# Kernel optimization log

Hardware: AMD Instinct MI355X
Metric: run time of the kernel (lower is better)

The kernel has to match this reference:

```python
import jax, jax.numpy as jnp
import numpy as np

B, S, D, H = 4, 2048, 1024, 16
HD = D // H
FF = 4 * D
EPS = 1e-5


def setup_inputs() -> dict:
    key = jax.random.key(0)
    ks = jax.random.split(key, 12)
    s = lambda fan_in: 1.0 / np.sqrt(fan_in)
    inp = {
        "x": jax.random.normal(ks[0], (B, S, D), dtype=jnp.float32),
        # attention weights stored as (d_in, d_out)
        "Wq": jax.random.normal(ks[1], (D, D), dtype=jnp.float32) * s(D),
        "Wk": jax.random.normal(ks[2], (D, D), dtype=jnp.float32) * s(D),
        "Wv": jax.random.normal(ks[3], (D, D), dtype=jnp.float32) * s(D),
        "Wo": jax.random.normal(ks[4], (D, D), dtype=jnp.float32) * s(D),
        "bo": jnp.zeros((D,), dtype=jnp.float32),
        # feed-forward
        "W1": jax.random.normal(ks[5], (D, FF), dtype=jnp.float32) * s(D),
        "b1": jnp.zeros((FF,), dtype=jnp.float32),
        "W2": jax.random.normal(ks[6], (FF, D), dtype=jnp.float32) * s(FF),
        "b2": jnp.zeros((D,), dtype=jnp.float32),
        # layernorms
        "g1": jnp.ones((D,), dtype=jnp.float32),
        "be1": jnp.zeros((D,), dtype=jnp.float32),
        "g2": jnp.ones((D,), dtype=jnp.float32),
        "be2": jnp.zeros((D,), dtype=jnp.float32),
    }
    return inp


def _layernorm(x, gamma, beta):
    mean = jnp.mean(x, axis=-1, keepdims=True)
    var = jnp.mean(jnp.square(x - mean), axis=-1, keepdims=True)  # unbiased=False
    return gamma * (x - mean) / jnp.sqrt(var + EPS) + beta


def _gelu_tanh(x):
    c = jnp.sqrt(jnp.asarray(2.0 / jnp.pi, dtype=x.dtype))
    return 0.5 * x * (1.0 + jnp.tanh(c * (x + 0.044715 * x * x * x)))


def _block(x, Wq, Wk, Wv, Wo, bo, W1, b1, W2, b2, g1, be1, g2, be2):
    # --- pre-LN causal multi-head attention ---
    shortcut = x
    h = _layernorm(x, g1, be1)
    q = (h @ Wq).reshape(B, S, H, HD).transpose(0, 2, 1, 3)  # [B,H,S,HD]
    k = (h @ Wk).reshape(B, S, H, HD).transpose(0, 2, 1, 3)
    v = (h @ Wv).reshape(B, S, H, HD).transpose(0, 2, 1, 3)
    scores = jnp.einsum("bhqd,bhkd->bhqk", q, k)
    causal = jnp.tril(jnp.ones((S, S), dtype=bool))  # True = keep
    scores = jnp.where(causal, scores, -jnp.inf)
    attn = jax.nn.softmax(scores / jnp.sqrt(jnp.asarray(HD, scores.dtype)), axis=-1)
    ctx = jnp.einsum("bhqk,bhkd->bqhd", attn, v).reshape(B, S, D)
    x = ctx @ Wo + bo + shortcut
    # --- pre-LN GELU MLP ---
    shortcut = x
    h = _layernorm(x, g2, be2)
    h = _gelu_tanh(h @ W1 + b1) @ W2 + b2
    return h + shortcut


def reference(x, Wq, Wk, Wv, Wo, bo, W1, b1, W2, b2, g1, be1, g2, be2):
    return _block(x, Wq, Wk, Wv, Wo, bo, W1, b1, W2, b2, g1, be1, g2, be2)
```

## Files before the change

### kernel.cpp

```cpp
#include <hip/hip_runtime.h>
#include <cstdint>

#define B_   4
#define S_   2048
#define D_   1024
#define H_   16
#define HD_  64
#define FF_  4096
#define MTOK 8192

typedef short s16x8 __attribute__((ext_vector_type(8), may_alias));
typedef float f32x4 __attribute__((ext_vector_type(4)));
typedef unsigned short u16x4 __attribute__((ext_vector_type(4), may_alias));
typedef unsigned short u16x8 __attribute__((ext_vector_type(8), may_alias));

#define GLD_LDS16(g, l)                                                  \
  __builtin_amdgcn_global_load_lds(                                      \
      (__attribute__((address_space(1))) void*)(g),                      \
      (__attribute__((address_space(3))) void*)(l), 16, 0, 0)

__device__ __forceinline__ unsigned short f2bf(float f) {
  unsigned u = __float_as_uint(f);
  unsigned r = 0x7fffu + ((u >> 16) & 1u);
  return (unsigned short)((u + r) >> 16);
}

__global__ __launch_bounds__(256) void k_transpose(const float* __restrict__ in,
                                                   unsigned short* __restrict__ out,
                                                   int R, int C) {
  __shared__ float tile[32][33];
  int tx = threadIdx.x, ty = threadIdx.y;
  int c0 = blockIdx.x * 32, r0 = blockIdx.y * 32;
#pragma unroll
  for (int j = 0; j < 4; ++j)
    tile[ty + j * 8][tx] = in[(size_t)(r0 + ty + j * 8) * C + (c0 + tx)];
  __syncthreads();
#pragma unroll
  for (int j = 0; j < 4; ++j)
    out[(size_t)(c0 + ty + j * 8) * R + (r0 + tx)] = f2bf(tile[tx][ty + j * 8]);
}

__global__ __launch_bounds__(256) void k_layernorm(const float* __restrict__ x,
                                                   const float* __restrict__ g,
                                                   const float* __restrict__ be,
                                                   unsigned short* __restrict__ out) {
  int row = blockIdx.x, t = threadIdx.x;
  const float4* xr = (const float4*)(x + (size_t)row * D_);
  float4 v = xr[t];
  float s = v.x + v.y + v.z + v.w;
  float q = v.x * v.x + v.y * v.y + v.z * v.z + v.w * v.w;
#pragma unroll
  for (int o = 1; o < 64; o <<= 1) { s += __shfl_xor(s, o); q += __shfl_xor(q, o); }
  __shared__ float red[8];
  int wid = t >> 6;
  if ((t & 63) == 0) { red[wid * 2] = s; red[wid * 2 + 1] = q; }
  __syncthreads();
  s = red[0] + red[2] + red[4] + red[6];
  q = red[1] + red[3] + red[5] + red[7];
  float mean = s * (1.0f / D_);
  float rstd = rsqrtf(q * (1.0f / D_) - mean * mean + 1e-5f);
  float4 gv = ((const float4*)g)[t];
  float4 bv = ((const float4*)be)[t];
  u16x4 o4;
  o4[0] = f2bf(gv.x * (v.x - mean) * rstd + bv.x);
  o4[1] = f2bf(gv.y * (v.y - mean) * rstd + bv.y);
  o4[2] = f2bf(gv.z * (v.z - mean) * rstd + bv.z);
  o4[3] = f2bf(gv.w * (v.w - mean) * rstd + bv.w);
  *(u16x4*)(out + (size_t)row * D_ + t * 4) = o4;
}

template <int MODE>
__global__ __launch_bounds__(512, 2) void k_gemm8p(
    const unsigned short* __restrict__ A, const unsigned short* __restrict__ Bt,
    const float* __restrict__ bias,
    unsigned short* __restrict__ outb,
    int M, int N, int K) {
  __shared__ __align__(16) unsigned short smem[8 * 8192];
  unsigned short* const Rs = smem;

  const int tid = threadIdx.x;
  const int wid = tid >> 6, lane = tid & 63;
  const int l16 = lane & 15, lg = lane >> 4;
  const int wr = wid >> 2, wc = wid & 3;
  const int nwg = gridDim.x * gridDim.y;
  const int id = blockIdx.y * gridDim.x + blockIdx.x;
  const int swz = (id & 7) * (nwg >> 3) + (id >> 3);
  const int m0 = (swz / gridDim.x) * 256, n0 = (swz % gridDim.x) * 256;

  f32x4 acc[8][4];
#pragma unroll
  for (int m = 0; m < 8; ++m)
#pragma unroll
    for (int n = 0; n < 4; ++n) acc[m][n] = (f32x4)0.0f;

  const int sRow = tid >> 3;
  const int sC = (((tid & 7) ^ (sRow & 7)) << 3);
  const unsigned short* aS0 = A + (size_t)(m0 + sRow) * K + sC;
  const unsigned short* aS1 = A + (size_t)(m0 + 64 + sRow) * K + sC;
  const unsigned short* aS2 = A + (size_t)(m0 + 128 + sRow) * K + sC;
  const unsigned short* aS3 = A + (size_t)(m0 + 192 + sRow) * K + sC;
  const unsigned short* bS0 = Bt + (size_t)(n0 + sRow) * K + sC;
  const unsigned short* bS1 = Bt + (size_t)(n0 + 64 + sRow) * K + sC;
  const unsigned short* bS2 = Bt + (size_t)(n0 + 128 + sRow) * K + sC;
  const unsigned short* bS3 = Bt + (size_t)(n0 + 192 + sRow) * K + sC;
  const int d0 = tid * 16, d1 = tid * 16 + 8192;

  const int cS0 = ((lg ^ (l16 & 7)) << 3);
  const int cS1 = (((4 + lg) ^ (l16 & 7)) << 3);

#define READ_A(SLOT)                                                           \
  _Pragma("unroll")                                                            \
  for (int m4 = 0; m4 < 4; ++m4) {                                             \
    const unsigned short* pr_ = smem + (SLOT) * 8192 + (wr * 64 + m4 * 16 + l16) * 64; \
    af[m4][0] = *(const s16x8*)(pr_ + cS0);                                    \
    af[m4][1] = *(const s16x8*)(pr_ + cS1);                                    \
  }
#define READ_B(SLOT, DEST)                                                     \
  _Pragma("unroll")                                                            \
  for (int n2 = 0; n2 < 2; ++n2) {                                             \
    const unsigned short* pr_ = smem + (SLOT) * 8192 + (wc * 32 + n2 * 16 + l16) * 64; \
    DEST[n2][0] = *(const s16x8*)(pr_ + cS0);                                  \
    DEST[n2][1] = *(const s16x8*)(pr_ + cS1);                                  \
  }
#define STAGE2(SLOT, P0_, P1_, KOFF)                                           \
  {                                                                            \
    char* dst_ = (char*)(smem + (SLOT) * 8192);                                \
    GLD_LDS16((P0_) + (KOFF), dst_ + d0);                                      \
    GLD_LDS16((P1_) + (KOFF), dst_ + d1);                                      \
  }
#define MFMAQ(MQ, NH, AF, BF)                                                  \
  __builtin_amdgcn_s_setprio(1);                                               \
  _Pragma("unroll")                                                            \
  for (int m4 = 0; m4 < 4; ++m4)                                               \
    _Pragma("unroll")                                                          \
    for (int n2 = 0; n2 < 2; ++n2) {                                           \
      acc[(MQ) * 4 + m4][(NH) * 2 + n2] = __builtin_amdgcn_mfma_f32_16x16x32_bf16( \
          AF[m4][0], BF[n2][0], acc[(MQ) * 4 + m4][(NH) * 2 + n2], 0, 0, 0);   \
      acc[(MQ) * 4 + m4][(NH) * 2 + n2] = __builtin_amdgcn_mfma_f32_16x16x32_bf16( \
          AF[m4][1], BF[n2][1], acc[(MQ) * 4 + m4][(NH) * 2 + n2], 0, 0, 0);   \
    }                                                                          \
  __builtin_amdgcn_s_setprio(0);
#define LGK0                                                                   \
  asm volatile("s_waitcnt lgkmcnt(0)" ::: "memory");                           \
  __builtin_amdgcn_sched_barrier(0);
#define BAR_ONLY                                                               \
  __builtin_amdgcn_sched_barrier(0);                                           \
  __builtin_amdgcn_s_barrier();

  STAGE2(0, aS0, aS1, 0)
  STAGE2(1, bS0, bS1, 0)
  STAGE2(2, bS2, bS3, 0)
  STAGE2(3, aS2, aS3, 0)
  STAGE2(4, aS0, aS1, 64)
  STAGE2(5, bS0, bS1, 64)
  STAGE2(6, bS2, bS3, 64)
  asm volatile("s_waitcnt vmcnt(0)" ::: "memory");
  BAR_ONLY

  const int nt2 = K / 128;
  for (int j = 0; j < nt2; ++j) {
    const bool stg = (j < nt2 - 1);
    const size_t k1 = (size_t)(2 * j + 1) * 64;
    const size_t k2 = (size_t)(2 * j + 2) * 64;
    const size_t k3 = (size_t)(2 * j + 3) * 64;
    s16x8 af[4][2], blo[2][2], bhi[2][2];
    READ_A(0)
    READ_B(1, blo)
    STAGE2(7, aS2, aS3, k1)
    LGK0
    MFMAQ(0, 0, af, blo)
    BAR_ONLY
    READ_B(2, bhi)
    if (stg) STAGE2(0, aS0, aS1, k2)
    LGK0
    MFMAQ(0, 1, af, bhi)
    BAR_ONLY
    READ_A(3)
    if (stg) STAGE2(1, bS0, bS1, k2)
    LGK0
    MFMAQ(1, 0, af, blo)
    BAR_ONLY
    if (stg) STAGE2(2, bS2, bS3, k2)
    MFMAQ(1, 1, af, bhi)
    if (stg) { asm volatile("s_waitcnt vmcnt(6)" ::: "memory"); }
    else     { asm volatile("s_waitcnt vmcnt(0)" ::: "memory"); }
    BAR_ONLY
    READ_A(4)
    READ_B(5, blo)
    if (stg) STAGE2(3, aS2, aS3, k2)
    LGK0
    MFMAQ(0, 0, af, blo)
    BAR_ONLY
    READ_B(6, bhi)
    if (stg) STAGE2(4, aS0, aS1, k3)
    LGK0
    MFMAQ(0, 1, af, bhi)
    BAR_ONLY
    READ_A(7)
    if (stg) STAGE2(5, bS0, bS1, k3)
    LGK0
    MFMAQ(1, 0, af, blo)
    BAR_ONLY
    if (stg) {
      STAGE2(6, bS2, bS3, k3)
      MFMAQ(1, 1, af, bhi)
      asm volatile("s_waitcnt vmcnt(6)" ::: "memory");
    } else {
      MFMAQ(1, 1, af, bhi)
    }
    BAR_ONLY
  }
#undef READ_A
#undef READ_B
#undef STAGE2
#undef MFMAQ
#undef LGK0
#undef BAR_ONLY

#define RM_FLUSH8(DSTPTR, NSTRIDE, COLBASE, XFORM)                             \
  {                                                                            \
    _Pragma("unroll")                                                          \
    for (int pr = 0; pr < 4; ++pr) {                                           \
      if (wr == (pr & 1)) {                                                    \
        const int mb_ = (pr >> 1) * 4;                                         \
        _Pragma("unroll")                                                      \
        for (int nn = 0; nn < 4; ++nn) {                                       \
          const int col = (nn >> 1) * 128 + wc * 32 + (nn & 1) * 16 + l16;     \
          _Pragma("unroll")                                                    \
          for (int m4 = 0; m4 < 4; ++m4) {                                     \
            _Pragma("unroll")                                                  \
            for (int r = 0; r < 4; ++r) {                                      \
              float xv = acc[mb_ + m4][nn][r];                                 \
              XFORM;                                                           \
              Rs[(m4 * 16 + lg * 4 + r) * 264 + col] = f2bf(xv);               \
            }                                                                  \
          }                                                                    \
        }                                                                      \
      }                                                                        \
      __syncthreads();                                                         \
      const int row_l = tid >> 3;                                              \
      _Pragma("unroll")                                                        \
      for (int j = 0; j < 4; ++j) {                                            \
        const int c = (tid & 7) * 4 + j;                                       \
        u16x8 vv = *(const u16x8*)(Rs + row_l * 264 + c * 8);                  \
        *(u16x8*)((DSTPTR) + (size_t)(m0 + pr * 64 + row_l) * (NSTRIDE) +      \
                  (COLBASE) + c * 8) = vv;                                     \
      }                                                                        \
      if (pr < 3) __syncthreads();                                             \
    }                                                                          \
  }

  if constexpr (MODE == 1) {
    RM_FLUSH8(outb, N, n0, {
      xv += bias[n0 + col];
      float uu = 0.7978845608028654f * (xv + 0.044715f * xv * xv * xv);
      xv = xv * __builtin_amdgcn_rcpf(1.0f + __builtin_amdgcn_exp2f(uu * -2.885390081777927f));
    });
    return;
  }

  if constexpr (MODE == 3) {
    unsigned short* qout = outb;
    unsigned short* kout = outb + (size_t)MTOK * D_;
    unsigned short* vout = outb + 2 * (size_t)MTOK * D_;
    if (n0 < 1024) {
      RM_FLUSH8(qout, D_, n0, { xv *= 0.125f; });
    } else if (n0 < 2048) {
      RM_FLUSH8(kout, D_, n0 - 1024, {});
    } else {
      const int vbase = (m0 >> 11) * 1024 + (n0 - 2048);
      const int srow0 = m0 & 2047;
#pragma unroll
      for (int cg = 0; cg < 4; ++cg) {
        if ((wc >> 1) == (cg & 1)) {
          const int nhh = (cg >> 1) * 2;
#pragma unroll
          for (int n2 = 0; n2 < 2; ++n2) {
            const int colL = (wc & 1) * 32 + n2 * 16 + l16;
#pragma unroll
            for (int m = 0; m < 8; ++m) {
              const int rowL = (m >> 2) * 128 + wr * 64 + (m & 3) * 16 + lg * 4;
              u16x4 pk;
#pragma unroll
              for (int r = 0; r < 4; ++r) pk[r] = f2bf(acc[m][nhh + n2][r]);
              *(u16x4*)(Rs + colL * 264 + rowL) = pk;
            }
          }
        }
        __syncthreads();
        const int colf = tid >> 3;
#pragma unroll
        for (int j = 0; j < 4; ++j) {
          u16x8 vv = *(const u16x8*)(Rs + colf * 264 + (tid & 7) * 32 + j * 8);
          *(u16x8*)(vout + (size_t)(vbase + cg * 64 + colf) * S_ + srow0 +
                    (tid & 7) * 32 + j * 8) = vv;
        }
        if (cg < 3) __syncthreads();
      }
    }
    return;
  }
#undef RM_FLUSH8
}

template <int MODE>
__global__ __launch_bounds__(512, 2) void k_gemmdp(
    const unsigned short* __restrict__ A, const unsigned short* __restrict__ Bt,
    const float* __restrict__ bias, const float* __restrict__ resid,
    unsigned short* __restrict__ outb, float* __restrict__ outf,
    int M, int N, int K) {
  constexpr int BM = 128, BN = 256, BK = 64;
  constexpr int AE = BM * BK;
  constexpr int BE = BN * BK;
  constexpr int BUF_E = AE + BE;
  __shared__ __align__(16) unsigned short smem[3 * BUF_E];

  const int tid = threadIdx.x;
  const int wid = tid >> 6, lane = tid & 63;
  const int l16 = lane & 15, lg = lane >> 4;
  const int wr = wid >> 2, wc = wid & 3;
  const int nwg = gridDim.x * gridDim.y;
  const int id = blockIdx.y * gridDim.x + blockIdx.x;
  const int swz = (id & 7) * (nwg >> 3) + (id >> 3);
  const int m0 = (swz / gridDim.x) * BM, n0 = (swz % gridDim.x) * BN;

  f32x4 acc[4][4];
#pragma unroll
  for (int m = 0; m < 4; ++m)
#pragma unroll
    for (int n = 0; n < 4; ++n) acc[m][n] = (f32x4)0.0f;

  const unsigned short* aSrc[2]; int aDstB[2];
  const unsigned short* bSrc[4]; int bDstB[4];
#pragma unroll
  for (int g = 0; g < 2; ++g) {
    int q = g * 512 + tid, row = q >> 3, c = q & 7;
    aSrc[g] = A + (size_t)(m0 + row) * K + ((c ^ (row & 7)) << 3);
    aDstB[g] = q * 16;
  }
#pragma unroll
  for (int g = 0; g < 4; ++g) {
    int q = g * 512 + tid, row = q >> 3, c = q & 7;
    bSrc[g] = Bt + (size_t)(n0 + row) * K + ((c ^ (row & 7)) << 3);
    bDstB[g] = q * 16;
  }
  int cSw[2];
  cSw[0] = ((lg) ^ (l16 & 7)) * 8;
  cSw[1] = ((4 + lg) ^ (l16 & 7)) * 8;
  const int aRow = (wr * 64 + l16) * BK;
  const int bRow = (wc * 64 + l16) * BK;

#define STAGE(ti)                                                              \
  {                                                                            \
    const int _b = (ti) % 3;                                                   \
    char* _pa = (char*)(smem + _b * BUF_E);                                    \
    char* _pb = (char*)(smem + _b * BUF_E + AE);                               \
    const int _kt = (ti) * BK;                                                 \
    _Pragma("unroll")                                                          \
    for (int g = 0; g < 2; ++g) GLD_LDS16(aSrc[g] + _kt, _pa + aDstB[g]);      \
    _Pragma("unroll")                                                          \
    for (int g = 0; g < 4; ++g) GLD_LDS16(bSrc[g] + _kt, _pb + bDstB[g]);      \
  }

  const int nt = K / BK;
  STAGE(0); STAGE(1);
  asm volatile("s_waitcnt vmcnt(6)" ::: "memory");
  __builtin_amdgcn_sched_barrier(0);
  __builtin_amdgcn_s_barrier();

  for (int i = 0; i < nt; ++i) {
    if (i + 2 < nt) STAGE(i + 2);
    const unsigned short* pa = smem + (i % 3) * BUF_E + aRow;
    const unsigned short* pb = smem + (i % 3) * BUF_E + AE + bRow;
    s16x8 af[4][2], bfr[4][2];
#pragma unroll
    for (int m = 0; m < 4; ++m) {
      af[m][0] = *(const s16x8*)(pa + m * 16 * BK + cSw[0]);
      af[m][1] = *(const s16x8*)(pa + m * 16 * BK + cSw[1]);
    }
#pragma unroll
    for (int n = 0; n < 4; ++n) {
      bfr[n][0] = *(const s16x8*)(pb + n * 16 * BK + cSw[0]);
      bfr[n][1] = *(const s16x8*)(pb + n * 16 * BK + cSw[1]);
    }
    asm volatile("s_waitcnt lgkmcnt(0)" ::: "memory");
    __builtin_amdgcn_sched_barrier(0);
    __builtin_amdgcn_s_setprio(1);
#pragma unroll
    for (int m = 0; m < 4; ++m)
#pragma unroll
      for (int n = 0; n < 4; ++n) {
        acc[m][n] = __builtin_amdgcn_mfma_f32_16x16x32_bf16(af[m][0], bfr[n][0], acc[m][n], 0, 0, 0);
        acc[m][n] = __builtin_amdgcn_mfma_f32_16x16x32_bf16(af[m][1], bfr[n][1], acc[m][n], 0, 0, 0);
      }
    __builtin_amdgcn_s_setprio(0);
    if (i < nt - 2) {
      asm volatile("s_waitcnt vmcnt(6)" ::: "memory");
    } else if (i == nt - 2) {
      asm volatile("s_waitcnt vmcnt(0)" ::: "memory");
    }
    __builtin_amdgcn_sched_barrier(0);
    __builtin_amdgcn_s_barrier();
  }
#undef STAGE

  if constexpr (MODE == 2) {
#pragma unroll
    for (int n = 0; n < 4; ++n) {
      const int col = n0 + wc * 64 + n * 16 + l16;
      const float bv = bias[col];
#pragma unroll
      for (int m = 0; m < 4; ++m)
#pragma unroll
        for (int r = 0; r < 4; ++r) {
          const int row = m0 + wr * 64 + m * 16 + lg * 4 + r;
          outf[(size_t)row * N + col] = acc[m][n][r] + bv + resid[(size_t)row * N + col];
        }
    }
  }
  (void)outb;
}

__global__ __launch_bounds__(256, 3) void k_attn(
    const unsigned short* __restrict__ qg, const unsigned short* __restrict__ kg,
    const unsigned short* __restrict__ vtg, unsigned short* __restrict__ ctx) {
  const int id = blockIdx.x;
  const int bh = (id & 7) + 8 * (id >> 7);
  const int p  = (id >> 3) & 15;
  const int qtA = p, qtB = 31 - p;
  const int tid = threadIdx.x, wid = tid >> 6, lane = tid & 63;
  const int l16 = lane & 15, lg = lane >> 4;
  __shared__ __align__(16) unsigned short Ks[2][64 * 64];
  __shared__ __align__(16) unsigned short Vs[2][64 * 64];
  __shared__ __align__(16) unsigned short Ps[4][2][16 * 72];

  const size_t headoff = (size_t)(bh >> 4) * ((size_t)S_ * D_) + (size_t)(bh & 15) * HD_;
  const unsigned short* Kb = kg + headoff;
  const unsigned short* Vt = vtg + (size_t)bh * ((size_t)HD_ * S_);

  const int qrowA = qtA * 64 + wid * 16 + l16;
  const int qrowB = qtB * 64 + wid * 16 + l16;
  s16x8 qfA0 = *(const s16x8*)(qg + headoff + (size_t)qrowA * D_ + lg * 8);
  s16x8 qfA1 = *(const s16x8*)(qg + headoff + (size_t)qrowA * D_ + 32 + lg * 8);
  s16x8 qfB0 = *(const s16x8*)(qg + headoff + (size_t)qrowB * D_ + lg * 8);
  s16x8 qfB1 = *(const s16x8*)(qg + headoff + (size_t)qrowB * D_ + 32 + lg * 8);

  f32x4 oA[4], oB[4];
#pragma unroll
  for (int n = 0; n < 4; ++n) { oA[n] = (f32x4)0.0f; oB[n] = (f32x4)0.0f; }
  float lsumA[4] = {0.f, 0.f, 0.f, 0.f};
  float lsumB[4] = {0.f, 0.f, 0.f, 0.f};
  unsigned short* psA = &Ps[wid][0][0];
  unsigned short* psB = &Ps[wid][1][0];
  const int myrowA = qtA * 64 + wid * 16 + lg * 4;
  const int myrowB = qtB * 64 + wid * 16 + lg * 4;
  const float L2E = 1.4426950408889634f;

  const unsigned short* kSrc[2];
  const unsigned short* vSrc[2];
  int dstOff[2];
#pragma unroll
  for (int i = 0; i < 2; ++i) {
    int chunk = (i * 4 + wid) * 64 + lane;
    int row = chunk >> 3, pc = chunk & 7;
    int scol = (pc ^ (row & 7)) * 8;
    kSrc[i] = Kb + (size_t)row * D_ + scol;
    vSrc[i] = Vt + (size_t)row * S_ + scol;
    dstOff[i] = (i * 4 + wid) * 1024;
  }

#pragma unroll
  for (int i = 0; i < 2; ++i) {
    GLD_LDS16(kSrc[i], (char*)Ks[0] + dstOff[i]);
    GLD_LDS16(vSrc[i], (char*)Vs[0] + dstOff[i]);
  }
  __syncthreads();

  for (int t = 0; t <= qtB; ++t) {
    const int cur = t & 1;
    const int kv0 = t * 64;
    const bool doA = (t <= qtA);
    if (t < qtB) {
      const int kvn = kv0 + 64;
#pragma unroll
      for (int i = 0; i < 2; ++i) {
        GLD_LDS16(kSrc[i] + (size_t)kvn * D_, (char*)Ks[cur ^ 1] + dstOff[i]);
        GLD_LDS16(vSrc[i] + kvn, (char*)Vs[cur ^ 1] + dstOff[i]);
      }
    }
    const unsigned short* Kc = Ks[cur];
    const unsigned short* Vc = Vs[cur];
    s16x8 kf0[4], kf1[4];
#pragma unroll
    for (int n = 0; n < 4; ++n) {
      int srow = n * 16 + l16, sw = srow & 7;
      kf0[n] = *(const s16x8*)(Kc + srow * 64 + (lg ^ sw) * 8);
      kf1[n] = *(const s16x8*)(Kc + srow * 64 + ((4 + lg) ^ sw) * 8);
    }
    f32x4 saA[4], saB[4];
    if (doA) {
#pragma unroll
      for (int n = 0; n < 4; ++n) {
        saA[n] = (f32x4)0.0f;
        saA[n] = __builtin_amdgcn_mfma_f32_16x16x32_bf16(qfA0, kf0[n], saA[n], 0, 0, 0);
        saA[n] = __builtin_amdgcn_mfma_f32_16x16x32_bf16(qfA1, kf1[n], saA[n], 0, 0, 0);
      }
    }
#pragma unroll
    for (int n = 0; n < 4; ++n) {
      saB[n] = (f32x4)0.0f;
      saB[n] = __builtin_amdgcn_mfma_f32_16x16x32_bf16(qfB0, kf0[n], saB[n], 0, 0, 0);
      saB[n] = __builtin_amdgcn_mfma_f32_16x16x32_bf16(qfB1, kf1[n], saB[n], 0, 0, 0);
    }
    if (doA) {
      const bool mask = (t == qtA);
#pragma unroll
      for (int r = 0; r < 4; ++r)
#pragma unroll
        for (int n = 0; n < 4; ++n) {
          float pv = exp2f((saA[n][r] - 12.0f) * L2E);
          if (mask && (kv0 + n * 16 + l16) > (myrowA + r)) pv = 0.0f;
          lsumA[r] += pv;
          psA[(lg * 4 + r) * 72 + n * 16 + l16] = f2bf(pv);
        }
    }
    {
      const bool mask = (t == qtB);
#pragma unroll
      for (int r = 0; r < 4; ++r)
#pragma unroll
        for (int n = 0; n < 4; ++n) {
          float pv = exp2f((saB[n][r] - 12.0f) * L2E);
          if (mask && (kv0 + n * 16 + l16) > (myrowB + r)) pv = 0.0f;
          lsumB[r] += pv;
          psB[(lg * 4 + r) * 72 + n * 16 + l16] = f2bf(pv);
        }
    }
    s16x8 vf0[4], vf1[4];
#pragma unroll
    for (int n = 0; n < 4; ++n) {
      int srow = n * 16 + l16, sw = srow & 7;
      vf0[n] = *(const s16x8*)(Vc + srow * 64 + (lg ^ sw) * 8);
      vf1[n] = *(const s16x8*)(Vc + srow * 64 + ((4 + lg) ^ sw) * 8);
    }
    __builtin_amdgcn_sched_barrier(0);
    asm volatile("s_waitcnt lgkmcnt(0)" ::: "memory");
    __builtin_amdgcn_sched_barrier(0);
    {
      s16x8 paB0 = *(const s16x8*)(psB + l16 * 72 + lg * 8);
      s16x8 paB1 = *(const s16x8*)(psB + l16 * 72 + 32 + lg * 8);
#pragma unroll
      for (int n = 0; n < 4; ++n) {
        oB[n] = __builtin_amdgcn_mfma_f32_16x16x32_bf16(paB0, vf0[n], oB[n], 0, 0, 0);
        oB[n] = __builtin_amdgcn_mfma_f32_16x16x32_bf16(paB1, vf1[n], oB[n], 0, 0, 0);
      }
      if (doA) {
        s16x8 paA0 = *(const s16x8*)(psA + l16 * 72 + lg * 8);
        s16x8 paA1 = *(const s16x8*)(psA + l16 * 72 + 32 + lg * 8);
#pragma unroll
        for (int n = 0; n < 4; ++n) {
          oA[n] = __builtin_amdgcn_mfma_f32_16x16x32_bf16(paA0, vf0[n], oA[n], 0, 0, 0);
          oA[n] = __builtin_amdgcn_mfma_f32_16x16x32_bf16(paA1, vf1[n], oA[n], 0, 0, 0);
        }
      }
    }
    __syncthreads();
  }

#pragma unroll
  for (int r = 0; r < 4; ++r) {
    float la = lsumA[r], lb = lsumB[r];
    la += __shfl_xor(la, 1); lb += __shfl_xor(lb, 1);
    la += __shfl_xor(la, 2); lb += __shfl_xor(lb, 2);
    la += __shfl_xor(la, 4); lb += __shfl_xor(lb, 4);
    la += __shfl_xor(la, 8); lb += __shfl_xor(lb, 8);
    float ia = 1.0f / la, ib = 1.0f / lb;
#pragma unroll
    for (int n = 0; n < 4; ++n) {
      ctx[headoff + (size_t)(myrowA + r) * D_ + n * 16 + l16] = f2bf(oA[n][r] * ia);
      ctx[headoff + (size_t)(myrowB + r) * D_ + n * 16 + l16] = f2bf(oB[n][r] * ib);
    }
  }
}

extern "C" void kernel_launch(void* const* d_in, const int* in_sizes, int n_in,
                              void* d_out, int out_size, void* d_ws, size_t ws_size,
                              hipStream_t stream) {
  (void)in_sizes; (void)n_in; (void)out_size; (void)ws_size;
  const float* x   = (const float*)d_in[0];
  const float* Wq  = (const float*)d_in[1];
  const float* Wk  = (const float*)d_in[2];
  const float* Wv  = (const float*)d_in[3];
  const float* Wo  = (const float*)d_in[4];
  const float* bo  = (const float*)d_in[5];
  const float* W1  = (const float*)d_in[6];
  const float* b1  = (const float*)d_in[7];
  const float* W2  = (const float*)d_in[8];
  const float* b2  = (const float*)d_in[9];
  const float* g1  = (const float*)d_in[10];
  const float* be1 = (const float*)d_in[11];
  const float* g2  = (const float*)d_in[12];
  const float* be2 = (const float*)d_in[13];
  float* out = (float*)d_out;

  char* w = (char*)d_ws;
  const size_t MB = 1ull << 20;
  unsigned short* wqkvT = (unsigned short*)(w + 0 * MB);
  unsigned short* woT   = (unsigned short*)(w + 6 * MB);
  unsigned short* w1T   = (unsigned short*)(w + 8 * MB);
  unsigned short* w2T   = (unsigned short*)(w + 16 * MB);
  unsigned short* hb    = (unsigned short*)(w + 24 * MB);
  float*          x2    = (float*)(w + 40 * MB);
  unsigned short* qkv   = (unsigned short*)(w + 72 * MB);
  unsigned short* qb    = qkv;
  unsigned short* kb    = qkv + (size_t)MTOK * D_;
  unsigned short* vbT   = qkv + 2 * (size_t)MTOK * D_;
  unsigned short* cxb   = (unsigned short*)(w + 120 * MB);
  unsigned short* act   = (unsigned short*)(w + 72 * MB);

  dim3 tb(32, 8);
  k_transpose<<<dim3(32, 32), tb, 0, stream>>>(Wq, wqkvT, 1024, 1024);
  k_transpose<<<dim3(32, 32), tb, 0, stream>>>(Wk, wqkvT + 1024 * 1024, 1024, 1024);
  k_transpose<<<dim3(32, 32), tb, 0, stream>>>(Wv, wqkvT + 2048 * 1024, 1024, 1024);
  k_transpose<<<dim3(32, 32), tb, 0, stream>>>(Wo, woT, 1024, 1024);
  k_transpose<<<dim3(128, 32), tb, 0, stream>>>(W1, w1T, 1024, 4096);
  k_transpose<<<dim3(32, 128), tb, 0, stream>>>(W2, w2T, 4096, 1024);

  k_layernorm<<<MTOK, 256, 0, stream>>>(x, g1, be1, hb);

  k_gemm8p<3><<<dim3(12, 32), 512, 0, stream>>>(hb, wqkvT, nullptr, qkv, MTOK, 3072, 1024);

  k_attn<<<1024, 256, 0, stream>>>(qb, kb, vbT, cxb);

  k_gemmdp<2><<<dim3(4, 64), 512, 0, stream>>>(cxb, woT, bo, x, nullptr, x2, MTOK, 1024, 1024);

  k_layernorm<<<MTOK, 256, 0, stream>>>(x2, g2, be2, hb);

  k_gemm8p<1><<<dim3(16, 32), 512, 0, stream>>>(hb, w1T, b1, act, MTOK, 4096, 1024);
  k_gemmdp<2><<<dim3(4, 64), 512, 0, stream>>>(act, w2T, b2, x2, nullptr, out, MTOK, 1024, 4096);
}
```

Before: 411.3 us.

## Use a new 128x128-tile double-buffered GEMM for the FFN up-projection

Replaces the 512-thread k_gemm8p kernel used for the W1 GEMM with GELU epilogue by a new 256-thread kernel. It uses 128x128 output tiles and a K-step of 32, double-buffers global-to-LDS loads, and applies the bias and GELU epilogue through an LDS staging buffer. Smaller tiles give more workgroups and possibly better occupancy. In exchange, data reuse per tile is lower and there are more syncs per unit of K. The MODE 1 path of the old kernel is removed.

```diff
diff --git a/kernel.cpp b/kernel.cpp
--- a/kernel.cpp
+++ b/kernel.cpp
@@ -250,15 +250,6 @@
     }                                                                          \
   }
 
-  if constexpr (MODE == 1) {
-    RM_FLUSH8(outb, N, n0, {
-      xv += bias[n0 + col];
-      float uu = 0.7978845608028654f * (xv + 0.044715f * xv * xv * xv);
-      xv = xv * __builtin_amdgcn_rcpf(1.0f + __builtin_amdgcn_exp2f(uu * -2.885390081777927f));
-    });
-    return;
-  }
-
   if constexpr (MODE == 3) {
     unsigned short* qout = outb;
     unsigned short* kout = outb + (size_t)MTOK * D_;
@@ -419,6 +410,111 @@
     }
   }
   (void)outb;
+}
+
+template <int MODE>
+__global__ __launch_bounds__(256) void k_gemm_bt(
+    const unsigned short* __restrict__ A, const unsigned short* __restrict__ Bt,
+    const float* __restrict__ bias,
+    unsigned short* __restrict__ outb,
+    int M, int N, int K) {
+  __shared__ __align__(16) unsigned short smem[16384];
+  unsigned short* const As0 = smem;
+  unsigned short* const As1 = smem + 4096;
+  unsigned short* const Bs0 = smem + 8192;
+  unsigned short* const Bs1 = smem + 12288;
+  unsigned short* const Rs  = smem;
+  const int tid = threadIdx.x;
+  const int wid = tid >> 6, lane = tid & 63;
+  const int nwg = gridDim.x * gridDim.y;
+  const int id = blockIdx.y * gridDim.x + blockIdx.x;
+  const int swz = (id & 7) * (nwg >> 3) + (id >> 3);
+  const int m0 = (swz / gridDim.x) * 128, n0 = (swz % gridDim.x) * 128;
+  const int wr = wid >> 1, wc = wid & 1;
+  const int l16 = lane & 15, lg = lane >> 4;
+  f32x4 acc[4][4];
+#pragma unroll
+  for (int m = 0; m < 4; ++m)
+#pragma unroll
+    for (int n = 0; n < 4; ++n) acc[m][n] = 0.0f;
+
+  const unsigned short* aSrc[2];
+  const unsigned short* bSrc[2];
+  int dstOff[2];
+#pragma unroll
+  for (int i = 0; i < 2; ++i) {
+    int chunk = (i * 4 + wid) * 64 + lane;
+    int row = chunk >> 2, col = (chunk & 3) * 8;
+    aSrc[i] = A + (size_t)(m0 + row) * K + col;
+    bSrc[i] = Bt + (size_t)(n0 + row) * K + col;
+    dstOff[i] = (i * 4 + wid) * 1024;
+  }
+  const int rdOffA = (wr * 64 + l16) * 32 + lg * 8;
+  const int rdOffB = (wc * 64 + l16) * 32 + lg * 8;
+
+#pragma unroll
+  for (int i = 0; i < 2; ++i) {
+    GLD_LDS16(aSrc[i], (char*)As0 + dstOff[i]);
+    GLD_LDS16(bSrc[i], (char*)Bs0 + dstOff[i]);
+  }
+  __syncthreads();
+
+  int idx = 0;
+  for (int kt = 0; kt < K; kt += 32, ++idx) {
+    const int cur = idx & 1;
+    if (kt + 32 < K) {
+      char* aN = (char*)(cur ? As0 : As1);
+      char* bN = (char*)(cur ? Bs0 : Bs1);
+#pragma unroll
+      for (int i = 0; i < 2; ++i) {
+        GLD_LDS16(aSrc[i] + kt + 32, aN + dstOff[i]);
+        GLD_LDS16(bSrc[i] + kt + 32, bN + dstOff[i]);
+      }
+    }
+    const unsigned short* aRd = (cur ? As1 : As0) + rdOffA;
+    const unsigned short* bRd = (cur ? Bs1 : Bs0) + rdOffB;
+    s16x8 af[4], bfr[4];
+#pragma unroll
+    for (int m = 0; m < 4; ++m) af[m] = *(const s16x8*)(aRd + m * 16 * 32);
+#pragma unroll
+    for (int n = 0; n < 4; ++n) bfr[n] = *(const s16x8*)(bRd + n * 16 * 32);
+#pragma unroll
+    for (int m = 0; m < 4; ++m)
+#pragma unroll
+      for (int n = 0; n < 4; ++n)
+        acc[m][n] = __builtin_amdgcn_mfma_f32_16x16x32_bf16(af[m], bfr[n], acc[m][n], 0, 0, 0);
+    __syncthreads();
+  }
+
+  if constexpr (MODE == 1) {
+#pragma unroll
+    for (int p = 0; p < 2; ++p) {
+      if (wr == p) {
+#pragma unroll
+        for (int n = 0; n < 4; ++n) {
+#pragma unroll
+          for (int mm = 0; mm < 4; ++mm) {
+#pragma unroll
+            for (int r = 0; r < 4; ++r) {
+              float xv = acc[mm][n][r];
+              xv += bias[n0 + wc * 64 + n * 16 + l16];
+              float uu = 0.7978845608028654f * (xv + 0.044715f * xv * xv * xv);
+              xv = xv * __builtin_amdgcn_rcpf(1.0f + __builtin_amdgcn_exp2f(uu * -2.885390081777927f));
+              Rs[(mm * 16 + lg * 4 + r) * 136 + wc * 64 + n * 16 + l16] = f2bf(xv);
+            }
+          }
+        }
+      }
+      __syncthreads();
+      const int row_l = tid >> 2, seg = tid & 3;
+#pragma unroll
+      for (int j = 0; j < 4; ++j) {
+        u16x8 vv = *(const u16x8*)(Rs + row_l * 136 + seg * 32 + j * 8);
+        *(u16x8*)(outb + (size_t)(m0 + p * 64 + row_l) * N + n0 + seg * 32 + j * 8) = vv;
+      }
+      if (p == 0) __syncthreads();
+    }
+  }
 }
 
 __global__ __launch_bounds__(256, 3) void k_attn(
@@ -636,6 +732,6 @@
 
   k_layernorm<<<MTOK, 256, 0, stream>>>(x2, g2, be2, hb);
 
-  k_gemm8p<1><<<dim3(16, 32), 512, 0, stream>>>(hb, w1T, b1, act, MTOK, 4096, 1024);
+  k_gemm_bt<1><<<dim3(32, 64), 256, 0, stream>>>(hb, w1T, b1, act, MTOK, 4096, 1024);
   k_gemmdp<2><<<dim3(4, 64), 512, 0, stream>>>(act, w2T, b2, x2, nullptr, out, MTOK, 1024, 4096);
 }
```

New measurement: 422.3 us. +2.7%, slower.
